# Kernel optimization log

Measured on AMD Instinct MI355X. Metric: run time of the kernel, lower is better.

## Reference

```python
import jax, jax.numpy as jnp
import numpy as np

B, C, IN, OUT = 256, 919, 400, 100

def setup_inputs() -> dict:
    key = jax.random.key(0)
    k1, k2 = jax.random.split(key)
    inputs = jax.random.normal(k1, (B, C, IN), dtype=jnp.float32)
    # glorot-style scaling for kernel
    kernel = jax.random.normal(k2, (1, C, IN, OUT), dtype=jnp.float32) * (1.0 / np.sqrt(IN))
    bias = jnp.zeros((1, C, OUT), dtype=jnp.float32)
    return {"inputs": inputs, "kernel": kernel, "bias": bias}

def reference(inputs, kernel, bias):
    # Original: broadcast (B,C,IN,1) * (1,C,IN,OUT), reduce over IN, add bias.
    # Equivalent fused form: per-category batched GEMM.
    # inputs: (B, C, IN); kernel: (1, C, IN, OUT) -> out: (B, C, OUT)
    out = jnp.einsum('bci,cio->bco', inputs, kernel[0])
    out = out + bias  # (1, C, OUT) broadcasts over batch
    return out  # activation is None (linear)
```

## Files before the change

### kernel.cpp

```cpp
#include <hip/hip_runtime.h>
#include <stdint.h>

#define NCAT  919
#define KDIM  400
#define NDIM  100
#define BK    32
#define NSTEP 13
#define KPAD  404
#define NROWS 100

typedef float  f32x4  __attribute__((ext_vector_type(4)));
typedef __bf16 bf16x8 __attribute__((ext_vector_type(8)));
typedef __bf16 bf16x2 __attribute__((ext_vector_type(2)));

__global__ void __launch_bounds__(512, 4)
cat_dense(const float* __restrict__ in, const float* __restrict__ wt,
          const float* __restrict__ bias, float* __restrict__ out)
{
  __shared__ __bf16 wlds[NROWS * KPAD];

  const int ob   = blockIdx.x;
  const int xcd  = ob & 7;
  const int bidx = ob >> 3;
  const int c    = (xcd < 7 ? xcd * 115 : 805 + (xcd - 7) * 114) + bidx;

  const int tid  = threadIdx.x;
  const int lane = tid & 63;
  const int wave = tid >> 6;
  const int rl   = lane & 15;
  const int kg   = (lane >> 4) * 8;

  const size_t rstride = (size_t)NCAT * KDIM;
  const float* gA0 = in + (size_t)c * KDIM + (size_t)(wave * 32 + rl) * rstride;
  const float* gA1 = gA0 + (size_t)16 * rstride;
  const float* gW  = wt + (size_t)c * (KDIM * NDIM);

  f32x4 areg[2][2][2];

#define LOADA(T) do {                                                      \
    const int kb_ = (T) * BK + kg;                                         \
    const int s_  = (T) & 1;                                               \
    if (kb_ + 8 <= KDIM) {     \
      areg[s_][0][0] = *(const f32x4*)(gA0 + kb_);                         \
      areg[s_][0][1] = *(const f32x4*)(gA0 + kb_ + 4);                     \
      areg[s_][1][0] = *(const f32x4*)(gA1 + kb_);                         \
      areg[s_][1][1] = *(const f32x4*)(gA1 + kb_ + 4);                     \
    } else {                                                               \
      areg[s_][0][0] = f32x4{0,0,0,0}; areg[s_][0][1] = f32x4{0,0,0,0};    \
      areg[s_][1][0] = f32x4{0,0,0,0}; areg[s_][1][1] = f32x4{0,0,0,0};    \
    }                                                                      \
  } while (0)

  LOADA(0);
  LOADA(1);

  #pragma unroll
  for (int i = 0; i < 10; ++i) {
    const int pc = tid + i * 512;
    if (pc < 5000) {
      const int kp = pc / 25;
      const int nq = pc - kp * 25;
      const int k  = kp * 2;
      const float* p = gW + (size_t)k * NDIM + nq * 4;
      const f32x4 w0 = *(const f32x4*)p;
      const f32x4 w1 = *(const f32x4*)(p + NDIM);
      #pragma unroll
      for (int j = 0; j < 4; ++j) {
        bf16x2 pk = { (__bf16)w0[j], (__bf16)w1[j] };
        *(bf16x2*)&wlds[(nq * 4 + j) * KPAD + k] = pk;
      }
    }
  }
  __syncthreads();

  f32x4 acc[2][7];
  #pragma unroll
  for (int m = 0; m < 2; ++m)
    #pragma unroll
    for (int n = 0; n < 7; ++n) acc[m][n] = f32x4{0, 0, 0, 0};

  #pragma unroll
  for (int t = 0; t < NSTEP; ++t) {
    const int pp = t & 1;
    bf16x8 a0, a1;
    #pragma unroll
    for (int j = 0; j < 4; ++j) {
      a0[j]     = (__bf16)areg[pp][0][0][j];
      a0[4 + j] = (__bf16)areg[pp][0][1][j];
      a1[j]     = (__bf16)areg[pp][1][0][j];
      a1[4 + j] = (__bf16)areg[pp][1][1][j];
    }
    if (t + 2 < NSTEP) LOADA(t + 2);
    const int kb2  = t * BK + kg;
    const int koff = (kb2 <= KDIM - 8) ? kb2 : (KDIM - 8);
    #pragma unroll
    for (int n = 0; n < 7; ++n) {
      const int brow = n * 16 + (n == 6 ? (rl & 3) : rl);
      bf16x8 b = *(const bf16x8*)&wlds[brow * KPAD + koff];
      acc[0][n] = __builtin_amdgcn_mfma_f32_16x16x32_bf16(a0, b, acc[0][n], 0, 0, 0);
      acc[1][n] = __builtin_amdgcn_mfma_f32_16x16x32_bf16(a1, b, acc[1][n], 0, 0, 0);
    }
  }

  const float* gB = bias + (size_t)c * NDIM;
  float* gO = out + (size_t)c * NDIM;
  #pragma unroll
  for (int n = 0; n < 7; ++n) {
    const int col = n * 16 + rl;
    if (col < NDIM) {
      const float bv = gB[col];
      #pragma unroll
      for (int m = 0; m < 2; ++m) {
        const int r0 = wave * 32 + m * 16 + (lane >> 4) * 4;
        #pragma unroll
        for (int j = 0; j < 4; ++j) {
          gO[(size_t)(r0 + j) * (NCAT * NDIM) + col] = acc[m][n][j] + bv;
        }
      }
    }
  }
}

extern "C" void kernel_launch(void* const* d_in, const int* in_sizes, int n_in,
                              void* d_out, int out_size, void* d_ws, size_t ws_size,
                              hipStream_t stream) {
  const float* in   = (const float*)d_in[0];
  const float* wt   = (const float*)d_in[1];
  const float* bias = (const float*)d_in[2];
  float* o          = (float*)d_out;
  cat_dense<<<dim3(NCAT), dim3(512), 0, stream>>>(in, wt, bias, o);
}
```

Measured before the change: 163.6 us.

## Make kernel persistent over categories with double-buffered weight LDS prefetch

Switches from one block per category to 256 persistent blocks, each looping over a contiguous range of about 3-4 categories. The next category's weights are staged through registers and converted into a second LDS buffer while MFMAs run on the current one, and A loads for the next category are issued early. The A register prefetch goes from two stages to four. This targets the exposed weight-load latency and the per-block startup cost, but it halves occupancy (launch bounds 4 to 2, doubled LDS) and leaves only 256 blocks, which can idle CUs and make the range split uneven.

```diff
diff --git a/kernel.cpp b/kernel.cpp
--- a/kernel.cpp
+++ b/kernel.cpp
@@ -1,28 +1,29 @@
 #include <hip/hip_runtime.h>
 #include <stdint.h>
 
-#define NCAT  919
-#define KDIM  400
-#define NDIM  100
-#define BK    32
-#define NSTEP 13
-#define KPAD  404
-#define NROWS 100
+#define NCAT   919
+#define KDIM   400
+#define NDIM   100
+#define BK     32
+#define NSTEP  13
+#define KPAD   408
+#define NROWS  100
+#define WELEM  (NROWS * KPAD)
 
 typedef float  f32x4  __attribute__((ext_vector_type(4)));
 typedef __bf16 bf16x8 __attribute__((ext_vector_type(8)));
 typedef __bf16 bf16x2 __attribute__((ext_vector_type(2)));
 
-__global__ void __launch_bounds__(512, 4)
+__global__ void __launch_bounds__(512, 2)
 cat_dense(const float* __restrict__ in, const float* __restrict__ wt,
           const float* __restrict__ bias, float* __restrict__ out)
 {
-  __shared__ __bf16 wlds[NROWS * KPAD];
+  __shared__ __bf16 wlds[2 * WELEM];
 
-  const int ob   = blockIdx.x;
-  const int xcd  = ob & 7;
-  const int bidx = ob >> 3;
-  const int c    = (xcd < 7 ? xcd * 115 : 805 + (xcd - 7) * 114) + bidx;
+  const int b0 = blockIdx.x;
+  const int bb = (b0 & 7) * 32 + (b0 >> 3);
+  int       c  = (bb * NCAT) >> 8;
+  const int ce = ((bb + 1) * NCAT) >> 8;
 
   const int tid  = threadIdx.x;
   const int lane = tid & 63;
@@ -31,93 +32,143 @@
   const int kg   = (lane >> 4) * 8;
 
   const size_t rstride = (size_t)NCAT * KDIM;
-  const float* gA0 = in + (size_t)c * KDIM + (size_t)(wave * 32 + rl) * rstride;
+  const size_t rowoff  = (size_t)(wave * 32 + rl) * rstride;
+
+  const float* gA0 = in + (size_t)c * KDIM + rowoff;
   const float* gA1 = gA0 + (size_t)16 * rstride;
-  const float* gW  = wt + (size_t)c * (KDIM * NDIM);
 
-  f32x4 areg[2][2][2];
+  f32x4 areg[4][2][2];
+  f32x4 wr0[5], wr1[5];
+  f32x4 acc[2][7];
 
-#define LOADA(T) do {                                                      \
-    const int kb_ = (T) * BK + kg;                                         \
-    const int s_  = (T) & 1;                                               \
-    if (kb_ + 8 <= KDIM) {     \
-      areg[s_][0][0] = *(const f32x4*)(gA0 + kb_);                         \
-      areg[s_][0][1] = *(const f32x4*)(gA0 + kb_ + 4);                     \
-      areg[s_][1][0] = *(const f32x4*)(gA1 + kb_);                         \
-      areg[s_][1][1] = *(const f32x4*)(gA1 + kb_ + 4);                     \
+#define LOADA_G(S, TT, A0, A1) do {                                        \
+    const int kb_ = (TT) * BK + kg;                                        \
+    if (kb_ + 8 <= KDIM) {        \
+      areg[S][0][0] = *(const f32x4*)((A0) + kb_);                         \
+      areg[S][0][1] = *(const f32x4*)((A0) + kb_ + 4);                     \
+      areg[S][1][0] = *(const f32x4*)((A1) + kb_);                         \
+      areg[S][1][1] = *(const f32x4*)((A1) + kb_ + 4);                     \
     } else {                                                               \
-      areg[s_][0][0] = f32x4{0,0,0,0}; areg[s_][0][1] = f32x4{0,0,0,0};    \
-      areg[s_][1][0] = f32x4{0,0,0,0}; areg[s_][1][1] = f32x4{0,0,0,0};    \
+      areg[S][0][0] = f32x4{0,0,0,0}; areg[S][0][1] = f32x4{0,0,0,0};      \
+      areg[S][1][0] = f32x4{0,0,0,0}; areg[S][1][1] = f32x4{0,0,0,0};      \
     }                                                                      \
   } while (0)
 
-  LOADA(0);
-  LOADA(1);
+#define WLOAD_HALF(H, GWP) do {                                            \
+    _Pragma("unroll")                                                      \
+    for (int i_ = 0; i_ < 5; ++i_) {                                       \
+      const int pc_ = tid + ((H) * 5 + i_) * 512;                          \
+      if (pc_ < 5000) {                                                    \
+        const int kp_ = pc_ / 25;                                          \
+        const int nq_ = pc_ - kp_ * 25;                                    \
+        const float* p_ = (GWP) + (size_t)(kp_ * 2) * NDIM + nq_ * 4;      \
+        wr0[i_] = *(const f32x4*)p_;                                       \
+        wr1[i_] = *(const f32x4*)(p_ + NDIM);                              \
+      }                                                                    \
+    }                                                                      \
+  } while (0)
 
-  #pragma unroll
-  for (int i = 0; i < 10; ++i) {
-    const int pc = tid + i * 512;
-    if (pc < 5000) {
-      const int kp = pc / 25;
-      const int nq = pc - kp * 25;
-      const int k  = kp * 2;
-      const float* p = gW + (size_t)k * NDIM + nq * 4;
-      const f32x4 w0 = *(const f32x4*)p;
-      const f32x4 w1 = *(const f32x4*)(p + NDIM);
-      #pragma unroll
-      for (int j = 0; j < 4; ++j) {
-        bf16x2 pk = { (__bf16)w0[j], (__bf16)w1[j] };
-        *(bf16x2*)&wlds[(nq * 4 + j) * KPAD + k] = pk;
-      }
-    }
+#define WWRITE_HALF(H, DST) do {                                           \
+    _Pragma("unroll")                                                      \
+    for (int i_ = 0; i_ < 5; ++i_) {                                       \
+      const int pc_ = tid + ((H) * 5 + i_) * 512;                          \
+      if (pc_ < 5000) {                                                    \
+        const int kp_ = pc_ / 25;                                          \
+        const int nq_ = pc_ - kp_ * 25;                                    \
+        const int k_  = kp_ * 2;                                           \
+        _Pragma("unroll")                                                  \
+        for (int j_ = 0; j_ < 4; ++j_) {                                   \
+          bf16x2 pk_ = { (__bf16)wr0[i_][j_], (__bf16)wr1[i_][j_] };       \
+          *(bf16x2*)&(DST)[(nq_ * 4 + j_) * KPAD + k_] = pk_;              \
+        }                                                                  \
+      }                                                                    \
+    }                                                                      \
+  } while (0)
+
+  LOADA_G(0, 0, gA0, gA1);
+  LOADA_G(1, 1, gA0, gA1);
+  LOADA_G(2, 2, gA0, gA1);
+  {
+    const float* gW = wt + (size_t)c * (KDIM * NDIM);
+    WLOAD_HALF(0, gW);  WWRITE_HALF(0, (&wlds[0]));
+    WLOAD_HALF(1, gW);  WWRITE_HALF(1, (&wlds[0]));
   }
   __syncthreads();
 
-  f32x4 acc[2][7];
   #pragma unroll
   for (int m = 0; m < 2; ++m)
     #pragma unroll
-    for (int n = 0; n < 7; ++n) acc[m][n] = f32x4{0, 0, 0, 0};
+    for (int n = 0; n < 7; ++n) acc[m][n] = f32x4{0,0,0,0};
 
-  #pragma unroll
-  for (int t = 0; t < NSTEP; ++t) {
-    const int pp = t & 1;
-    bf16x8 a0, a1;
+  for (int it = 0; ; ++it) {
+    const bool hasnext = (c + 1 < ce);
+    const int  cn      = hasnext ? c + 1 : c;
+    const float* gA0n  = in + (size_t)cn * KDIM + rowoff;
+    const float* gA1n  = gA0n + (size_t)16 * rstride;
+    const float* gWn   = wt + (size_t)cn * (KDIM * NDIM);
+    const __bf16* R    = &wlds[(it & 1) * WELEM];
+    __bf16*       Wb   = &wlds[((it & 1) ^ 1) * WELEM];
+
+    if (hasnext) WLOAD_HALF(0, gWn);
+
     #pragma unroll
-    for (int j = 0; j < 4; ++j) {
-      a0[j]     = (__bf16)areg[pp][0][0][j];
-      a0[4 + j] = (__bf16)areg[pp][0][1][j];
-      a1[j]     = (__bf16)areg[pp][1][0][j];
-      a1[4 + j] = (__bf16)areg[pp][1][1][j];
+    for (int t = 0; t < NSTEP; ++t) {
+      const int pp = t & 3;
+      bf16x8 a0, a1;
+      #pragma unroll
+      for (int j = 0; j < 4; ++j) {
+        a0[j]     = (__bf16)areg[pp][0][0][j];
+        a0[4 + j] = (__bf16)areg[pp][0][1][j];
+        a1[j]     = (__bf16)areg[pp][1][0][j];
+        a1[4 + j] = (__bf16)areg[pp][1][1][j];
+      }
+      if (t <= 9)               LOADA_G((t + 3) & 3, t + 3, gA0, gA1);
+      if (t == 6 && hasnext) { WWRITE_HALF(0, Wb); WLOAD_HALF(1, gWn); }
+      if (t == 10 && hasnext) { LOADA_G(1, 1, gA0n, gA1n);
+                                LOADA_G(2, 2, gA0n, gA1n); }
+      if (t == 12 && hasnext) { LOADA_G(0, 0, gA0n, gA1n); }
+
+      const int kb2  = t * BK + kg;
+      const int koff = (kb2 <= KDIM - 8) ? kb2 : (KDIM - 8);
+      #pragma unroll
+      for (int n = 0; n < 7; ++n) {
+        const int brow = n * 16 + (n == 6 ? (rl & 3) : rl);
+        bf16x8 b = *(const bf16x8*)&R[brow * KPAD + koff];
+        acc[0][n] = __builtin_amdgcn_mfma_f32_16x16x32_bf16(a0, b, acc[0][n], 0,0,0);
+        acc[1][n] = __builtin_amdgcn_mfma_f32_16x16x32_bf16(a1, b, acc[1][n], 0,0,0);
+      }
     }
-    if (t + 2 < NSTEP) LOADA(t + 2);
-    const int kb2  = t * BK + kg;
-    const int koff = (kb2 <= KDIM - 8) ? kb2 : (KDIM - 8);
-    #pragma unroll
-    for (int n = 0; n < 7; ++n) {
-      const int brow = n * 16 + (n == 6 ? (rl & 3) : rl);
-      bf16x8 b = *(const bf16x8*)&wlds[brow * KPAD + koff];
-      acc[0][n] = __builtin_amdgcn_mfma_f32_16x16x32_bf16(a0, b, acc[0][n], 0, 0, 0);
-      acc[1][n] = __builtin_amdgcn_mfma_f32_16x16x32_bf16(a1, b, acc[1][n], 0, 0, 0);
+
+    if (hasnext) {
+      WWRITE_HALF(1, Wb);
+      __syncthreads();
     }
-  }
 
-  const float* gB = bias + (size_t)c * NDIM;
-  float* gO = out + (size_t)c * NDIM;
-  #pragma unroll
-  for (int n = 0; n < 7; ++n) {
-    const int col = n * 16 + rl;
-    if (col < NDIM) {
-      const float bv = gB[col];
+    {
+      const float* gB = bias + (size_t)c * NDIM;
+      float* gO = out + (size_t)c * NDIM;
       #pragma unroll
-      for (int m = 0; m < 2; ++m) {
-        const int r0 = wave * 32 + m * 16 + (lane >> 4) * 4;
-        #pragma unroll
-        for (int j = 0; j < 4; ++j) {
-          gO[(size_t)(r0 + j) * (NCAT * NDIM) + col] = acc[m][n][j] + bv;
+      for (int n = 0; n < 7; ++n) {
+        const int col = n * 16 + rl;
+        if (col < NDIM) {
+          const float bv = gB[col];
+          #pragma unroll
+          for (int m = 0; m < 2; ++m) {
+            const int r0 = wave * 32 + m * 16 + (lane >> 4) * 4;
+            #pragma unroll
+            for (int j = 0; j < 4; ++j)
+              gO[(size_t)(r0 + j) * ((size_t)NCAT * NDIM) + col] = acc[m][n][j] + bv;
+          }
         }
       }
     }
+
+    if (!hasnext) break;
+    #pragma unroll
+    for (int m = 0; m < 2; ++m)
+      #pragma unroll
+      for (int n = 0; n < 7; ++n) acc[m][n] = f32x4{0,0,0,0};
+    gA0 = gA0n; gA1 = gA1n; c = cn;
   }
 }
 
@@ -128,5 +179,5 @@
   const float* wt   = (const float*)d_in[1];
   const float* bias = (const float*)d_in[2];
   float* o          = (float*)d_out;
-  cat_dense<<<dim3(NCAT), dim3(512), 0, stream>>>(in, wt, bias, o);
+  cat_dense<<<dim3(256), dim3(512), 0, stream>>>(in, wt, bias, o);
 }
```

After: 269.0 us. 64.4% more time.
